# Kernel tuning notes

Hardware: AMD Instinct MI355X
Metric: run time of the kernel (lower is better)

Reference implementation:

```python
import jax, jax.numpy as jnp
import numpy as np
from jax import lax

# 8-neighbor zero-pad offsets as (left, right, top, bottom), matching nn.ZeroPad2d args
PADS = [(0, 2, 0, 2), (1, 1, 0, 2), (2, 0, 0, 2), (0, 2, 1, 1),
        (2, 0, 1, 1), (0, 2, 2, 0), (1, 1, 2, 0), (2, 0, 2, 0)]
BN_EPS = 1e-5


def conv2d(x, w, pad):
    return lax.conv_general_dilated(x, w, (1, 1), [(pad, pad), (pad, pad)],
                                    dimension_numbers=('NCHW', 'OIHW', 'NCHW'))


def batchnorm(x, gamma, beta, mean, var):
    inv = gamma * lax.rsqrt(var + BN_EPS)
    return x * inv[None, :, None, None] + (beta - mean * inv)[None, :, None, None]


def resize_bilinear(x, oh, ow):
    # F.interpolate(mode='bilinear', align_corners=False)
    n, c, h, w = x.shape
    ys = jnp.clip((jnp.arange(oh, dtype=x.dtype) + 0.5) * (h / oh) - 0.5, 0.0, None)
    xs = jnp.clip((jnp.arange(ow, dtype=x.dtype) + 0.5) * (w / ow) - 0.5, 0.0, None)
    y0 = jnp.floor(ys); x0 = jnp.floor(xs)
    wy = (ys - y0)[:, None]; wx = (xs - x0)[None, :]
    y0i = jnp.clip(y0.astype(jnp.int32), 0, h - 1)
    y1i = jnp.clip(y0i + 1, 0, h - 1)
    x0i = jnp.clip(x0.astype(jnp.int32), 0, w - 1)
    x1i = jnp.clip(x0i + 1, 0, w - 1)
    r0 = x[:, :, y0i, :]; r1 = x[:, :, y1i, :]
    top = r0[:, :, :, x0i] * (1 - wx) + r0[:, :, :, x1i] * wx
    bot = r1[:, :, :, x0i] * (1 - wx) + r1[:, :, :, x1i] * wx
    return top * (1 - wy) + bot * wy


def lrwarp_error(left, disp, right):
    # Warp right image toward left using horizontal disparity (bilinear,
    # zero padding outside), then per-channel absolute photometric error.
    n, c, h, w = right.shape
    xs = jnp.arange(w, dtype=disp.dtype)[None, None, None, :] - disp  # [n,1,h,w]
    x0 = jnp.floor(xs)
    frac = xs - x0
    x0i = x0.astype(jnp.int32)
    x1i = x0i + 1
    v0 = ((x0i >= 0) & (x0i < w)).astype(right.dtype)
    v1 = ((x1i >= 0) & (x1i < w)).astype(right.dtype)
    x0c = jnp.broadcast_to(jnp.clip(x0i, 0, w - 1), (n, c, h, w))
    x1c = jnp.broadcast_to(jnp.clip(x1i, 0, w - 1), (n, c, h, w))
    g0 = jnp.take_along_axis(right, x0c, axis=3) * v0
    g1 = jnp.take_along_axis(right, x1c, axis=3) * v1
    warped = g0 * (1 - frac) + g1 * frac
    return jnp.abs(left - warped)


def setup_inputs() -> dict:
    key = jax.random.key(0)
    ks = jax.random.split(key, 16)
    N, H, W = 8, 256, 256
    inp = {
        'normal_estimation': jax.random.normal(ks[0], (N, 3, H, W), jnp.float32),
        'left_image': jax.random.uniform(ks[1], (N, 3, 512, 512), jnp.float32),
        'right_image': jax.random.uniform(ks[2], (N, 3, 512, 512), jnp.float32),
        'coarse_disparity': jax.random.uniform(ks[3], (N, 1, H, W), jnp.float32),
        'w1': jax.random.normal(ks[4], (32, 12, 3, 3), jnp.float32) * 0.1,
        'g1': jnp.ones((32,), jnp.float32), 'b1': jnp.zeros((32,), jnp.float32),
        'm1': jax.random.normal(ks[5], (32,), jnp.float32) * 0.01,
        'v1': jax.random.uniform(ks[6], (32,), jnp.float32, 0.5, 1.5),
        'w2': jax.random.normal(ks[7], (64, 32, 3, 3), jnp.float32) * 0.1,
        'g2': jnp.ones((64,), jnp.float32), 'b2': jnp.zeros((64,), jnp.float32),
        'm2': jax.random.normal(ks[8], (64,), jnp.float32) * 0.01,
        'v2': jax.random.uniform(ks[9], (64,), jnp.float32, 0.5, 1.5),
        'w3': jax.random.normal(ks[10], (8, 64, 1, 1), jnp.float32) * 0.1,
    }
    return inp


def _forward(normal_estimation, left_image, right_image, coarse_disparity,
             w1, g1, b1, m1, v1, w2, g2, b2, m2, v2, w3):
    H, W = coarse_disparity.shape[-2], coarse_disparity.shape[-1]
    cur_l = resize_bilinear(left_image, H, W)
    cur_r = resize_bilinear(right_image, H, W)
    disp_err = lrwarp_error(cur_l, coarse_disparity, cur_r)
    feats = jnp.concatenate([normal_estimation, cur_l, cur_r, disp_err], axis=1)
    x = jax.nn.relu(batchnorm(conv2d(feats, w1, 1), g1, b1, m1, v1))
    x = jax.nn.relu(batchnorm(conv2d(x, w2, 1), g2, b2, m2, v2))
    aff = jax.nn.relu(conv2d(x, w3, 0))  # [N,8,H,W]
    gate_p = jnp.stack([jnp.pad(aff[:, k], ((0, 0), (t, b), (l, r)))
                        for k, (l, r, t, b) in enumerate(PADS)], axis=1)
    d = coarse_disparity[:, 0]
    disp_p = jnp.stack([jnp.pad(d, ((0, 0), (t, b), (l, r)))
                        for (l, r, t, b) in PADS], axis=1)
    gate = jax.nn.softmax(gate_p, axis=1)
    prop = jnp.sum(gate * disp_p, axis=1, keepdims=True)[:, :, 1:-1, 1:-1]
    return prop * 0.3 + coarse_disparity * 0.7


def reference(normal_estimation, left_image, right_image, coarse_disparity,
              w1, g1, b1, m1, v1, w2, g2, b2, m2, v2, w3):
    return _forward(normal_estimation, left_image, right_image, coarse_disparity,
                    w1, g1, b1, m1, v1, w2, g2, b2, m2, v2, w3)
```

## Files before the change

### kernel.cpp

```cpp
#include <hip/hip_runtime.h>
#include <math.h>

#define NB 8
#define HH 256
#define WW 256
#define HW (HH*WW)

#define OFF_AFFB  0UL
#define OFF_W1FB  8388608UL
#define OFF_B1FB  8400896UL
#define OFF_W2FB  8401024UL
#define OFF_B2FB  8437888UL
#define OFF_W3FB  8438144UL
#define OFF_FEATS 8440192UL

typedef short  short8 __attribute__((ext_vector_type(8)));
typedef ushort u16x8  __attribute__((ext_vector_type(8)));
typedef ushort u16x4  __attribute__((ext_vector_type(4)));
typedef float  f32x4  __attribute__((ext_vector_type(4)));

__device__ __forceinline__ ushort f2bf(float x) {
  uint u = __float_as_uint(x);
  return (ushort)((u + 0x7FFFu + ((u >> 16) & 1u)) >> 16);
}
__device__ __forceinline__ float bf2f(ushort h) {
  uint u = ((uint)h) << 16;
  return __uint_as_float(u);
}

__global__ __launch_bounds__(256) void feats_row(
    const float* __restrict__ normal, const float* __restrict__ left,
    const float* __restrict__ right, const float* __restrict__ disp,
    const float* __restrict__ w1, const float* __restrict__ g1,
    const float* __restrict__ b1, const float* __restrict__ m1,
    const float* __restrict__ v1,
    const float* __restrict__ w2, const float* __restrict__ g2,
    const float* __restrict__ b2, const float* __restrict__ m2,
    const float* __restrict__ v2, const float* __restrict__ w3,
    char* __restrict__ wsb) {
  if (blockIdx.x >= 2048) {
    int idx = (blockIdx.x - 2048) * 256 + threadIdx.x;
    ushort* w1f = (ushort*)(wsb + OFF_W1FB);
    float* b1f  = (float*)(wsb + OFF_B1FB);
    ushort* w2f = (ushort*)(wsb + OFF_W2FB);
    float* b2f  = (float*)(wsb + OFF_B2FB);
    ushort* w3f = (ushort*)(wsb + OFF_W3FB);
    if (idx < 6144) {
      int jj = idx & 7;
      int lane = (idx >> 3) & 63;
      int nt = (idx >> 9) & 1;
      int s = idx >> 10;
      int ky = s >> 1, t = s & 1;
      int q = lane >> 4, lx = lane & 15;
      int k = q * 8 + jj;
      int dcol = k >> 4, ch = k & 15;
      int kx = t * 2 + dcol;
      int out = nt * 16 + lx;
      float inv = g1[out] / sqrtf(v1[out] + 1e-5f);
      float val = (ch < 12 && kx < 3) ? w1[((out * 12 + ch) * 3 + ky) * 3 + kx] * inv : 0.f;
      w1f[idx] = f2bf(val);
    }
    int j = idx - 6144;
    if (j >= 0 && j < 18432) {
      int kk   = j >> 11;
      int nt   = (j >> 9) & 3;
      int lane = (j >> 3) & 63;
      int jj   = j & 7;
      int q  = lane >> 4, lx = lane & 15;
      int cin = q * 8 + jj;
      int out = nt * 16 + lx;
      float inv = g2[out] / sqrtf(v2[out] + 1e-5f);
      w2f[j] = f2bf(w2[(out * 32 + cin) * 9 + kk] * inv);
      if (kk == 0 && q == 0 && jj == 0) b2f[out] = b2[out] - m2[out] * inv;
    }
    int k2 = idx - 24576;
    if (k2 >= 0 && k2 < 32) {
      float inv = g1[k2] / sqrtf(v1[k2] + 1e-5f);
      b1f[k2] = b1[k2] - m1[k2] * inv;
    }
    int k3 = idx - 24608;
    if (k3 >= 0 && k3 < 1024) {
      int jj = k3 & 7;
      int lane = (k3 >> 3) & 63;
      int slice = k3 >> 9;
      int q = lane >> 4, lx = lane & 15;
      int ch = slice * 32 + q * 8 + jj;
      w3f[k3] = (lx < 8) ? f2bf(w3[lx * 64 + ch]) : (ushort)0;
    }
    return;
  }
  __shared__ float curR[3][256];
  int blk = blockIdx.x;
  int n = blk >> 8;
  int i = blk & 255;
  int j = threadIdx.x;
  int i2 = i << 1;
  ushort* feats = (ushort*)(wsb + OFF_FEATS);
  float cl[3], cr[3];
#pragma unroll
  for (int c = 0; c < 3; ++c) {
    const float* Lp = left + ((size_t)(n * 3 + c) * 512 + i2) * 512 + (j << 1);
    float2 a0 = *(const float2*)Lp;
    float2 a1 = *(const float2*)(Lp + 512);
    cl[c] = 0.25f * (a0.x + a0.y + a1.x + a1.y);
    const float* Rp = right + ((size_t)(n * 3 + c) * 512 + i2) * 512 + (j << 1);
    float2 b0 = *(const float2*)Rp;
    float2 b1v = *(const float2*)(Rp + 512);
    cr[c] = 0.25f * (b0.x + b0.y + b1v.x + b1v.y);
    curR[c][j] = cr[c];
  }
  float nm[3];
#pragma unroll
  for (int c = 0; c < 3; ++c)
    nm[c] = normal[(size_t)(n * 3 + c) * HW + i * WW + j];
  float d = disp[(size_t)n * HW + i * WW + j];
  __syncthreads();
  float xs = (float)j - d;
  float x0f = floorf(xs);
  float fr = xs - x0f;
  int ix0 = (int)x0f;
  int ix1 = ix0 + 1;
  float vm0 = (ix0 >= 0 && ix0 < WW) ? 1.f : 0.f;
  float vm1 = (ix1 >= 0 && ix1 < WW) ? 1.f : 0.f;
  int x0c = min(max(ix0, 0), WW - 1);
  int x1c = min(max(ix1, 0), WW - 1);
  ushort tmp[16];
#pragma unroll
  for (int c = 0; c < 3; ++c) {
    float warped = curR[c][x0c] * vm0 * (1.f - fr) + curR[c][x1c] * vm1 * fr;
    tmp[9 + c] = f2bf(fabsf(cl[c] - warped));
    tmp[c] = f2bf(nm[c]);
    tmp[3 + c] = f2bf(cl[c]);
    tmp[6 + c] = f2bf(cr[c]);
  }
#pragma unroll
  for (int c = 12; c < 16; ++c) tmp[c] = 0;
  size_t ob = ((size_t)((n << 16) + i * WW + j)) * 16;
  *(u16x8*)&feats[ob] = *(u16x8*)&tmp[0];
  *(u16x8*)&feats[ob + 8] = *(u16x8*)&tmp[8];
}

__global__ __launch_bounds__(256) void trunk_kernel(char* __restrict__ wsb) {
  __shared__ ushort buf[18304];
  ushort* x1t = buf + 6464;
  const short8* __restrict__ w1fv = (const short8*)(wsb + OFF_W1FB);
  const float* __restrict__ b1f = (const float*)(wsb + OFF_B1FB);
  const short8* __restrict__ w2fv = (const short8*)(wsb + OFF_W2FB);
  const float* __restrict__ b2f = (const float*)(wsb + OFF_B2FB);
  const short8* __restrict__ w3fv = (const short8*)(wsb + OFF_W3FB);
  const ushort* __restrict__ feats = (const ushort*)(wsb + OFF_FEATS);
  ushort* aff = (ushort*)(wsb + OFF_AFFB);

  int blk = blockIdx.x;
  int n = blk >> 8;
  int t = blk & 255;
  int ty0 = (t >> 4) << 4;
  int tx0 = (t & 15) << 4;
  int tid = threadIdx.x;
  int lane = tid & 63;
  int wid = tid >> 6;
  int q = lane >> 4;
  int lx = lane & 15;

  if (tid < 8) *(u16x8*)&buf[(800 + tid) * 8] = (u16x8)0;
  for (int e = tid; e < 800; e += 256) {
    int row = e / 40;
    int rem = e - row * 40;
    int col = rem >> 1;
    int cc = rem & 1;
    int gy = ty0 + row - 2, gx = tx0 + col - 2;
    u16x8 v = (u16x8)0;
    if (gy >= 0 && gy < HH && gx >= 0 && gx < WW)
      v = *(const u16x8*)&feats[((size_t)((n << 16) + gy * WW + gx)) * 16 + cc * 8];
    int slot = e ^ ((e >> 3) & 7);
    *(u16x8*)&buf[slot * 8] = v;
  }
  __syncthreads();

  {
    short8 bw1[6][2];
#pragma unroll
    for (int s = 0; s < 6; ++s)
#pragma unroll
      for (int nt = 0; nt < 2; ++nt) bw1[s][nt] = w1fv[(s * 2 + nt) * 64 + lane];
    float bias1[2] = {b1f[lx], b1f[16 + lx]};
    for (int m = wid; m < 21; m += 4) {
      int pidx = min(m * 16 + lx, 323);
      int oyr = pidx / 18, oxr = pidx - oyr * 18;
      f32x4 a1[2];
      a1[0] = (f32x4)0.f; a1[1] = (f32x4)0.f;
#pragma unroll
      for (int s = 0; s < 6; ++s) {
        int ky = s >> 1, tt = s & 1;
        int G = ((oyr + ky) * 20 + oxr + tt * 2 + (q >> 1)) * 2 + (q & 1);
        int slot = G ^ ((G >> 3) & 7);
        short8 a = *(const short8*)&buf[slot * 8];
        a1[0] = __builtin_amdgcn_mfma_f32_16x16x32_bf16(a, bw1[s][0], a1[0], 0, 0, 0);
        a1[1] = __builtin_amdgcn_mfma_f32_16x16x32_bf16(a, bw1[s][1], a1[1], 0, 0, 0);
      }
#pragma unroll
      for (int r = 0; r < 4; ++r) {
        int p2 = m * 16 + q * 4 + r;
        if (p2 < 324) {
          int ry = p2 / 18, rx = p2 - ry * 18;
          int gy = ty0 + ry - 1, gx = tx0 + rx - 1;
          bool okp = (gy >= 0 && gy < HH && gx >= 0 && gx < WW);
#pragma unroll
          for (int nt = 0; nt < 2; ++nt) {
            float v = okp ? fmaxf(a1[nt][r] + bias1[nt], 0.f) : 0.f;
            x1t[(ry * 18 + rx) * 36 + nt * 16 + lx] = f2bf(v);
          }
        }
      }
    }
  }
  __syncthreads();

  f32x4 acc[4][4];
#pragma unroll
  for (int mt = 0; mt < 4; ++mt)
#pragma unroll
    for (int nt = 0; nt < 4; ++nt) acc[mt][nt] = (f32x4)0.f;
#pragma unroll
  for (int kk = 0; kk < 9; ++kk) {
    int ky = kk / 3, kx = kk - ky * 3;
    short8 a[4], b[4];
#pragma unroll
    for (int mt = 0; mt < 4; ++mt) {
      int row = wid * 4 + mt;
      a[mt] = *(const short8*)&x1t[((row + ky) * 18 + lx + kx) * 36 + q * 8];
    }
#pragma unroll
    for (int nt = 0; nt < 4; ++nt) b[nt] = w2fv[(kk * 4 + nt) * 64 + lane];
#pragma unroll
    for (int mt = 0; mt < 4; ++mt)
#pragma unroll
      for (int nt = 0; nt < 4; ++nt)
        acc[mt][nt] = __builtin_amdgcn_mfma_f32_16x16x32_bf16(a[mt], b[nt], acc[mt][nt], 0, 0, 0);
  }
  __syncthreads();

#pragma unroll
  for (int nt = 0; nt < 4; ++nt) {
    float bias = b2f[nt * 16 + lx];
#pragma unroll
    for (int mt = 0; mt < 4; ++mt) {
      int row = wid * 4 + mt;
#pragma unroll
      for (int r = 0; r < 4; ++r) {
        int p = row * 16 + q * 4 + r;
        float v = fmaxf(acc[mt][nt][r] + bias, 0.f);
        buf[p * 68 + nt * 16 + lx] = f2bf(v);
      }
    }
  }
  __syncthreads();

  short8 bw3[2];
  bw3[0] = w3fv[lane];
  bw3[1] = w3fv[64 + lane];
  f32x4 acc3[4];
#pragma unroll
  for (int mt = 0; mt < 4; ++mt) acc3[mt] = (f32x4)0.f;
#pragma unroll
  for (int mt = 0; mt < 4; ++mt) {
    int p = wid * 64 + mt * 16 + lx;
#pragma unroll
    for (int s = 0; s < 2; ++s) {
      short8 a3 = *(const short8*)&buf[p * 68 + s * 32 + q * 8];
      acc3[mt] = __builtin_amdgcn_mfma_f32_16x16x32_bf16(a3, bw3[s], acc3[mt], 0, 0, 0);
    }
  }
  if (lx < 8) {
#pragma unroll
    for (int mt = 0; mt < 4; ++mt) {
      int py = ty0 + wid * 4 + mt;
      int px = tx0 + q * 4;
      u16x4 pk;
#pragma unroll
      for (int r = 0; r < 4; ++r) pk[r] = f2bf(fmaxf(acc3[mt][r], 0.f));
      *(u16x4*)&aff[((size_t)(n * 8 + lx)) * HW + (size_t)py * WW + px] = pk;
    }
  }
}

__global__ __launch_bounds__(256) void final_kernel(const float* __restrict__ disp,
                                                    const char* __restrict__ wsb,
                                                    float* __restrict__ out) {
  int gid = blockIdx.x * 256 + threadIdx.x;
  int n = gid >> 14;
  int r = gid & 16383;
  int i = r >> 6;
  int j0 = (r & 63) << 2;
  const ushort* aff = (const ushort*)(wsb + OFF_AFFB);
  float d6[3][6];
#pragma unroll
  for (int rr = 0; rr < 3; ++rr) {
    int y = min(max(i + rr - 1, 0), HH - 1);
    const float* dp = disp + (size_t)n * HW + y * WW;
    float4 c4 = *(const float4*)(dp + j0);
    d6[rr][1] = c4.x; d6[rr][2] = c4.y; d6[rr][3] = c4.z; d6[rr][4] = c4.w;
    d6[rr][0] = dp[max(j0 - 1, 0)];
    d6[rr][5] = dp[min(j0 + 4, WW - 1)];
  }
  const int dy[8] = {1, 1, 1, 0, 0, -1, -1, -1};
  const int dx[8] = {1, 0, -1, 1, -1, 1, 0, -1};
  float g[8][4], dvv[8][4];
#pragma unroll
  for (int k = 0; k < 8; ++k) {
    int y = i + dy[k];
    bool vy = (y >= 0 && y < HH);
    int yc = min(max(y, 0), HH - 1);
    const ushort* ap = aff + ((size_t)(n * 8 + k)) * HW + (size_t)yc * WW;
    float w6[6];
    u16x4 c4 = *(const u16x4*)(ap + j0);
    w6[1] = bf2f(c4[0]); w6[2] = bf2f(c4[1]); w6[3] = bf2f(c4[2]); w6[4] = bf2f(c4[3]);
    w6[0] = bf2f(ap[max(j0 - 1, 0)]);
    w6[5] = bf2f(ap[min(j0 + 4, WW - 1)]);
    int rr = dy[k] + 1;
#pragma unroll
    for (int p = 0; p < 4; ++p) {
      int xp = j0 + p + dx[k];
      bool ok = vy && (xp >= 0) && (xp < WW);
      g[k][p] = ok ? w6[p + 1 + dx[k]] : 0.f;
      dvv[k][p] = ok ? d6[rr][p + 1 + dx[k]] : 0.f;
    }
  }
  float4 res;
#pragma unroll
  for (int p = 0; p < 4; ++p) {
    float m = g[0][p];
#pragma unroll
    for (int k = 1; k < 8; ++k) m = fmaxf(m, g[k][p]);
    float se = 0.f, sed = 0.f;
#pragma unroll
    for (int k = 0; k < 8; ++k) {
      float e = __expf(g[k][p] - m);
      se += e;
      sed += e * dvv[k][p];
    }
    float dc = d6[1][p + 1];
    (&res.x)[p] = 0.3f * (sed / se) + 0.7f * dc;
  }
  *(float4*)(out + (size_t)n * HW + i * WW + j0) = res;
}

extern "C" void kernel_launch(void* const* d_in, const int* in_sizes, int n_in,
                              void* d_out, int out_size, void* d_ws, size_t ws_size,
                              hipStream_t stream) {
  const float* normal = (const float*)d_in[0];
  const float* left   = (const float*)d_in[1];
  const float* right  = (const float*)d_in[2];
  const float* disp   = (const float*)d_in[3];
  const float* w1 = (const float*)d_in[4];
  const float* g1 = (const float*)d_in[5];
  const float* b1 = (const float*)d_in[6];
  const float* m1 = (const float*)d_in[7];
  const float* v1 = (const float*)d_in[8];
  const float* w2 = (const float*)d_in[9];
  const float* g2 = (const float*)d_in[10];
  const float* b2 = (const float*)d_in[11];
  const float* m2 = (const float*)d_in[12];
  const float* v2 = (const float*)d_in[13];
  const float* w3 = (const float*)d_in[14];
  char* wsb  = (char*)d_ws;
  float* out = (float*)d_out;

  hipLaunchKernelGGL(feats_row, dim3(2149), dim3(256), 0, stream,
                     normal, left, right, disp,
                     w1, g1, b1, m1, v1, w2, g2, b2, m2, v2, w3, wsb);
  hipLaunchKernelGGL(trunk_kernel, dim3(2048), dim3(256), 0, stream, wsb);
  hipLaunchKernelGGL(final_kernel, dim3(512), dim3(256), 0, stream, disp, wsb, out);
}
```

Before: 165.7 us.

## Use packed bf16 conversion, permuted channel layouts, and interior-tile fast path in trunk

Replaces the software f32-to-bf16 rounding with the hardware v_cvt_pk_bf16_f32 instruction, packing two values per store. Permutes the input-channel order of the conv2 and conv3 weights so that conv1 and conv2 outputs can be written to shared memory as packed 32-bit or 64-bit words instead of scattered 16-bit stores. Restructures the conv1 M-tiling so whole 18-wide rows map to the first 18 tiles, with separate halo tiles. Adds an interior-tile fast path that skips bounds checks. This adds complexity and depends on the permutations staying consistent between the weight prep and the trunk kernel.

After: 166.2 us. About the same (+0.3%).

```diff
diff --git a/kernel.cpp b/kernel.cpp
--- a/kernel.cpp
+++ b/kernel.cpp
@@ -26,6 +26,11 @@
 __device__ __forceinline__ float bf2f(ushort h) {
   uint u = ((uint)h) << 16;
   return __uint_as_float(u);
+}
+__device__ __forceinline__ uint pk2bf(float a, float b) {
+  uint r;
+  asm("v_cvt_pk_bf16_f32 %0, %1, %2" : "=v"(r) : "v"(a), "v"(b));
+  return r;
 }
 
 __global__ __launch_bounds__(256) void feats_row(
@@ -67,7 +72,8 @@
       int lane = (j >> 3) & 63;
       int jj   = j & 7;
       int q  = lane >> 4, lx = lane & 15;
-      int cin = q * 8 + jj;
+      int cs = q * 8 + jj;
+      int cin = ((cs & 1) << 4) | (cs >> 1);
       int out = nt * 16 + lx;
       float inv = g2[out] / sqrtf(v2[out] + 1e-5f);
       w2f[j] = f2bf(w2[(out * 32 + cin) * 9 + kk] * inv);
@@ -84,8 +90,9 @@
       int lane = (k3 >> 3) & 63;
       int slice = k3 >> 9;
       int q = lane >> 4, lx = lane & 15;
-      int ch = slice * 32 + q * 8 + jj;
-      w3f[k3] = (lx < 8) ? f2bf(w3[lx * 64 + ch]) : (ushort)0;
+      int cs = slice * 32 + q * 8 + jj;
+      int chp = ((cs & 3) << 4) | (cs >> 2);
+      w3f[k3] = (lx < 8) ? f2bf(w3[lx * 64 + chp]) : (ushort)0;
     }
     return;
   }
@@ -124,25 +131,29 @@
   float vm1 = (ix1 >= 0 && ix1 < WW) ? 1.f : 0.f;
   int x0c = min(max(ix0, 0), WW - 1);
   int x1c = min(max(ix1, 0), WW - 1);
-  ushort tmp[16];
+  float tv[16];
 #pragma unroll
   for (int c = 0; c < 3; ++c) {
     float warped = curR[c][x0c] * vm0 * (1.f - fr) + curR[c][x1c] * vm1 * fr;
-    tmp[9 + c] = f2bf(fabsf(cl[c] - warped));
-    tmp[c] = f2bf(nm[c]);
-    tmp[3 + c] = f2bf(cl[c]);
-    tmp[6 + c] = f2bf(cr[c]);
-  }
-#pragma unroll
-  for (int c = 12; c < 16; ++c) tmp[c] = 0;
+    tv[9 + c] = fabsf(cl[c] - warped);
+    tv[c] = nm[c];
+    tv[3 + c] = cl[c];
+    tv[6 + c] = cr[c];
+  }
+  uint pk[8];
+#pragma unroll
+  for (int k = 0; k < 6; ++k) pk[k] = pk2bf(tv[2 * k], tv[2 * k + 1]);
+  pk[6] = 0u;
+  pk[7] = 0u;
   size_t ob = ((size_t)((n << 16) + i * WW + j)) * 16;
-  *(u16x8*)&feats[ob] = *(u16x8*)&tmp[0];
-  *(u16x8*)&feats[ob + 8] = *(u16x8*)&tmp[8];
+  *(uint4*)&feats[ob] = make_uint4(pk[0], pk[1], pk[2], pk[3]);
+  *(uint4*)&feats[ob + 8] = make_uint4(pk[4], pk[5], pk[6], pk[7]);
 }
 
 __global__ __launch_bounds__(256) void trunk_kernel(char* __restrict__ wsb) {
   __shared__ ushort buf[18304];
   ushort* x1t = buf + 6464;
+  uint*   x1u = (uint*)x1t;
   const short8* __restrict__ w1fv = (const short8*)(wsb + OFF_W1FB);
   const float* __restrict__ b1f = (const float*)(wsb + OFF_B1FB);
   const short8* __restrict__ w2fv = (const short8*)(wsb + OFF_W2FB);
@@ -161,19 +172,31 @@
   int wid = tid >> 6;
   int q = lane >> 4;
   int lx = lane & 15;
+  bool border = (ty0 == 0) || (ty0 == 240) || (tx0 == 0) || (tx0 == 240);
 
   if (tid < 8) *(u16x8*)&buf[(800 + tid) * 8] = (u16x8)0;
-  for (int e = tid; e < 800; e += 256) {
-    int row = e / 40;
-    int rem = e - row * 40;
-    int col = rem >> 1;
-    int cc = rem & 1;
-    int gy = ty0 + row - 2, gx = tx0 + col - 2;
-    u16x8 v = (u16x8)0;
-    if (gy >= 0 && gy < HH && gx >= 0 && gx < WW)
-      v = *(const u16x8*)&feats[((size_t)((n << 16) + gy * WW + gx)) * 16 + cc * 8];
-    int slot = e ^ ((e >> 3) & 7);
-    *(u16x8*)&buf[slot * 8] = v;
+  if (!border) {
+    for (int e = tid; e < 800; e += 256) {
+      int row = e / 40;
+      int rem = e - row * 40;
+      int gy = ty0 + row - 2, gx = tx0 + (rem >> 1) - 2;
+      u16x8 v = *(const u16x8*)&feats[((size_t)((n << 16) + gy * WW + gx)) * 16 + (rem & 1) * 8];
+      int slot = e ^ ((e >> 3) & 7);
+      *(u16x8*)&buf[slot * 8] = v;
+    }
+  } else {
+    for (int e = tid; e < 800; e += 256) {
+      int row = e / 40;
+      int rem = e - row * 40;
+      int col = rem >> 1;
+      int cc = rem & 1;
+      int gy = ty0 + row - 2, gx = tx0 + col - 2;
+      u16x8 v = (u16x8)0;
+      if (gy >= 0 && gy < HH && gx >= 0 && gx < WW)
+        v = *(const u16x8*)&feats[((size_t)((n << 16) + gy * WW + gx)) * 16 + cc * 8];
+      int slot = e ^ ((e >> 3) & 7);
+      *(u16x8*)&buf[slot * 8] = v;
+    }
   }
   __syncthreads();
 
@@ -184,31 +207,60 @@
 #pragma unroll
       for (int nt = 0; nt < 2; ++nt) bw1[s][nt] = w1fv[(s * 2 + nt) * 64 + lane];
     float bias1[2] = {b1f[lx], b1f[16 + lx]};
+    int laneoff = (lx << 1) + ((q >> 1) << 1) + (q & 1);
+    int colbT = 32 + ((lx & 1) << 1) + ((q >> 1) << 1) + (q & 1);
+    int rowT = lx >> 1;
     for (int m = wid; m < 21; m += 4) {
-      int pidx = min(m * 16 + lx, 323);
-      int oyr = pidx / 18, oxr = pidx - oyr * 18;
       f32x4 a1[2];
-      a1[0] = (f32x4)0.f; a1[1] = (f32x4)0.f;
+      a1[0] = (f32x4)0.f;
+      a1[1] = (f32x4)0.f;
+      int tb = m - 18;
+      int Gb;
+      if (m < 18) Gb = m * 40 + laneoff;
+      else        Gb = min(tb * 8 + rowT, 17) * 40 + colbT;
 #pragma unroll
       for (int s = 0; s < 6; ++s) {
-        int ky = s >> 1, tt = s & 1;
-        int G = ((oyr + ky) * 20 + oxr + tt * 2 + (q >> 1)) * 2 + (q & 1);
+        int G = Gb + (s >> 1) * 40 + (s & 1) * 4;
         int slot = G ^ ((G >> 3) & 7);
         short8 a = *(const short8*)&buf[slot * 8];
         a1[0] = __builtin_amdgcn_mfma_f32_16x16x32_bf16(a, bw1[s][0], a1[0], 0, 0, 0);
         a1[1] = __builtin_amdgcn_mfma_f32_16x16x32_bf16(a, bw1[s][1], a1[1], 0, 0, 0);
       }
-#pragma unroll
-      for (int r = 0; r < 4; ++r) {
-        int p2 = m * 16 + q * 4 + r;
-        if (p2 < 324) {
-          int ry = p2 / 18, rx = p2 - ry * 18;
-          int gy = ty0 + ry - 1, gx = tx0 + rx - 1;
-          bool okp = (gy >= 0 && gy < HH && gx >= 0 && gx < WW);
-#pragma unroll
-          for (int nt = 0; nt < 2; ++nt) {
-            float v = okp ? fmaxf(a1[nt][r] + bias1[nt], 0.f) : 0.f;
-            x1t[(ry * 18 + rx) * 36 + nt * 16 + lx] = f2bf(v);
+      if (m < 18) {
+        int base = (m * 18 + (q << 2)) * 18 + lx;
+        if (!border) {
+#pragma unroll
+          for (int r = 0; r < 4; ++r) {
+            float v0 = fmaxf(a1[0][r] + bias1[0], 0.f);
+            float v1 = fmaxf(a1[1][r] + bias1[1], 0.f);
+            x1u[base + r * 18] = pk2bf(v0, v1);
+          }
+        } else {
+          bool gyok = (unsigned)(ty0 + m - 1) < 256u;
+          int gx0 = tx0 - 1 + (q << 2);
+#pragma unroll
+          for (int r = 0; r < 4; ++r) {
+            bool ok = gyok && ((unsigned)(gx0 + r) < 256u);
+            float v0 = ok ? fmaxf(a1[0][r] + bias1[0], 0.f) : 0.f;
+            float v1 = ok ? fmaxf(a1[1][r] + bias1[1], 0.f) : 0.f;
+            x1u[base + r * 18] = pk2bf(v0, v1);
+          }
+        }
+      } else {
+#pragma unroll
+        for (int r = 0; r < 4; ++r) {
+          int io = (q << 2) + r;
+          int hy = tb * 8 + (io >> 1);
+          int hx = 16 + (io & 1);
+          if (hy < 18) {
+            float v0 = fmaxf(a1[0][r] + bias1[0], 0.f);
+            float v1 = fmaxf(a1[1][r] + bias1[1], 0.f);
+            if (border) {
+              bool ok = ((unsigned)(ty0 + hy - 1) < 256u) && ((unsigned)(tx0 + hx - 1) < 256u);
+              v0 = ok ? v0 : 0.f;
+              v1 = ok ? v1 : 0.f;
+            }
+            x1u[(hy * 18 + hx) * 18 + lx] = pk2bf(v0, v1);
           }
         }
       }
@@ -238,20 +290,23 @@
       for (int nt = 0; nt < 4; ++nt)
         acc[mt][nt] = __builtin_amdgcn_mfma_f32_16x16x32_bf16(a[mt], b[nt], acc[mt][nt], 0, 0, 0);
   }
+  float bias2q[4] = {b2f[lx], b2f[16 + lx], b2f[32 + lx], b2f[48 + lx]};
   __syncthreads();
 
 #pragma unroll
-  for (int nt = 0; nt < 4; ++nt) {
-    float bias = b2f[nt * 16 + lx];
-#pragma unroll
-    for (int mt = 0; mt < 4; ++mt) {
-      int row = wid * 4 + mt;
-#pragma unroll
-      for (int r = 0; r < 4; ++r) {
-        int p = row * 16 + q * 4 + r;
-        float v = fmaxf(acc[mt][nt][r] + bias, 0.f);
-        buf[p * 68 + nt * 16 + lx] = f2bf(v);
-      }
+  for (int mt = 0; mt < 4; ++mt) {
+    int row = wid * 4 + mt;
+#pragma unroll
+    for (int r = 0; r < 4; ++r) {
+      int p = row * 16 + (q << 2) + r;
+      float c0 = fmaxf(acc[mt][0][r] + bias2q[0], 0.f);
+      float c1 = fmaxf(acc[mt][1][r] + bias2q[1], 0.f);
+      float c2 = fmaxf(acc[mt][2][r] + bias2q[2], 0.f);
+      float c3 = fmaxf(acc[mt][3][r] + bias2q[3], 0.f);
+      uint2 pv;
+      pv.x = pk2bf(c0, c1);
+      pv.y = pk2bf(c2, c3);
+      *(uint2*)&buf[p * 68 + (lx << 2)] = pv;
     }
   }
   __syncthreads();
@@ -275,11 +330,11 @@
 #pragma unroll
     for (int mt = 0; mt < 4; ++mt) {
       int py = ty0 + wid * 4 + mt;
-      int px = tx0 + q * 4;
-      u16x4 pk;
-#pragma unroll
-      for (int r = 0; r < 4; ++r) pk[r] = f2bf(fmaxf(acc3[mt][r], 0.f));
-      *(u16x4*)&aff[((size_t)(n * 8 + lx)) * HW + (size_t)py * WW + px] = pk;
+      int px = tx0 + (q << 2);
+      uint2 pv;
+      pv.x = pk2bf(fmaxf(acc3[mt][0], 0.f), fmaxf(acc3[mt][1], 0.f));
+      pv.y = pk2bf(fmaxf(acc3[mt][2], 0.f), fmaxf(acc3[mt][3], 0.f));
+      *(uint2*)&aff[((size_t)(n * 8 + lx)) * HW + (size_t)py * WW + px] = pv;
     }
   }
 }
```
